# Kernel tuning notes

Hardware: AMD Instinct MI355X
Metric: run time of the kernel (lower is better)

The kernel has to match this reference:

```python
import jax, jax.numpy as jnp
import numpy as np

B, T = 256, 2048
K_LABELS = 50
K2 = K_LABELS + 2  # includes START (K) and STOP (K+1) tags
NEG_INF = -10000.0


def setup_inputs() -> dict:
    key = jax.random.key(0)
    k1, k2, k3, k4 = jax.random.split(key, 4)
    emissions = jax.random.normal(k1, (B, T, K2), dtype=jnp.float32)
    transitions = jax.random.normal(k2, (K2, K2), dtype=jnp.float32)
    lengths = jax.random.randint(k3, (B,), 1, T + 1, dtype=jnp.int64)
    labels = jax.random.randint(k4, (B, T), 0, K_LABELS, dtype=jnp.int64)
    return {"emissions": emissions, "transitions": transitions,
            "lengths": lengths, "labels": labels}


def _forward_algo(emissions, transitions, lengths):
    b, t, k2 = emissions.shape
    start_tag, stop_tag = k2 - 2, k2 - 1
    init = jnp.full((k2,), NEG_INF, emissions.dtype).at[start_tag].set(0.0)
    alpha0 = jnp.broadcast_to(init, (b, k2))  # [B, K2]

    def step(alpha, emit):
        # tag_var[b, next, prev] = emit[b, next] + trans[next, prev] + alpha[b, prev]
        tag_var = emit[:, :, None] + transitions[None, :, :] + alpha[:, None, :]
        new_alpha = jax.nn.logsumexp(tag_var, axis=2)  # [B, K2]
        return new_alpha, new_alpha

    _, alphas = jax.lax.scan(step, alpha0, jnp.swapaxes(emissions, 0, 1))
    all_alphas = jnp.concatenate([alpha0[None], alphas], axis=0)  # [T+1, B, K2]
    fv = all_alphas[lengths, jnp.arange(b)]  # alpha at each sequence's final step
    terminal = fv + transitions[stop_tag][None, :]
    return jax.nn.logsumexp(terminal, axis=1)  # [B]


def _score_label(emissions, transitions, lengths, labels):
    b, t, k2 = emissions.shape
    start_tag, stop_tag = k2 - 2, k2 - 1
    start_col = jnp.full((b, 1), start_tag, labels.dtype)
    stop_col = jnp.full((b, 1), stop_tag, labels.dtype)
    pad_start = jnp.concatenate([start_col, labels], axis=1)  # [B, T+1]
    pad_stop = jnp.concatenate([labels, stop_col], axis=1)    # [B, T+1]
    pos = jnp.arange(t + 1)
    pad_stop = jnp.where(pos[None, :] >= lengths[:, None], stop_tag, pad_stop)
    # transition score over positions 0..length (inclusive)
    trans_mask = pos[None, :] <= lengths[:, None]
    trans_sc = jnp.where(trans_mask, transitions[pad_stop, pad_start], 0.0).sum(axis=1)
    # emission score over positions 0..length-1
    emit_mask = jnp.arange(t)[None, :] < lengths[:, None]
    emit_vals = jnp.take_along_axis(emissions, labels[..., None], axis=-1)[..., 0]
    emit_sc = jnp.where(emit_mask, emit_vals, 0.0).sum(axis=1)
    return trans_sc + emit_sc  # [B]


def reference(emissions, transitions, lengths, labels):
    forward_score = _forward_algo(emissions, transitions, lengths)
    gold_score = _score_label(emissions, transitions, lengths, labels)
    return jnp.mean(forward_score - gold_score)
```

## Files before the change

### kernel.cpp

```cpp
#include <hip/hip_runtime.h>


#define B_    256
#define T_    2048
#define K2_   52
#define LOG2E_ 1.4426950408889634f
#define LN2_   0.6931471805599453f

__device__ __forceinline__ float rdlane(float v, int src) {
  return __uint_as_float(__builtin_amdgcn_readlane(__float_as_uint(v), src));
}
__device__ __forceinline__ int imin(int a, int b) { return a < b ? a : b; }
__device__ __forceinline__ int imax(int a, int b) { return a > b ? a : b; }

#define FORALL52(F) \
  F(0,0) F(1,1) F(2,2) F(3,3) F(4,0) F(5,1) F(6,2) F(7,3) \
  F(8,0) F(9,1) F(10,2) F(11,3) F(12,0) F(13,1) F(14,2) F(15,3) \
  F(16,0) F(17,1) F(18,2) F(19,3) F(20,0) F(21,1) F(22,2) F(23,3) \
  F(24,0) F(25,1) F(26,2) F(27,3) F(28,0) F(29,1) F(30,2) F(31,3) \
  F(32,0) F(33,1) F(34,2) F(35,3) F(36,0) F(37,1) F(38,2) F(39,3) \
  F(40,0) F(41,1) F(42,2) F(43,3) F(48,0) F(49,1) F(50,2) F(51,3) \
  F(44,0) F(45,1) F(46,2) F(47,3)

#define DECLM_F(i, c) float M_##i = __builtin_amdgcn_exp2f(tr[n * K2_ + i] * LOG2E_);
#define DECLM_B(i, c) float M_##i = __builtin_amdgcn_exp2f(tr[i * K2_ + n] * LOG2E_);
#define ACCF(i, c)  _a##c = fmaf(M_##i, rdlane(_src, i), _a##c);

#define MATVEC(OUTY) \
    float _a0 = 0.0f, _a1 = 0.0f, _a2 = 0.0f, _a3 = 0.0f; \
    FORALL52(ACCF) \
    float OUTY = (_a0 + _a1) + (_a2 + _a3);

#define FSTEP_R(EV, NEWIDX) do {                                \
    float _ne  = emb[(NEWIDX) * K2_ + n];                       \
    float _m   = rdlane(vv, 50);                                \
    float _inv = __builtin_amdgcn_rcpf(_m);                     \
    C += __builtin_amdgcn_logf(_m);                             \
    float _E = __builtin_amdgcn_exp2f((EV) * LOG2E_);           \
    float _src = vv;                                            \
    MATVEC(_y)                                                  \
    vv = _y * _inv * _E;                                        \
    EV = _ne;                                                   \
  } while (0)
#define FSTEP_N(EV, NEWIDX) do {                                \
    float _ne  = emb[(NEWIDX) * K2_ + n];                       \
    float _E = __builtin_amdgcn_exp2f((EV) * LOG2E_);           \
    float _src = vv;                                            \
    MATVEC(_y)                                                  \
    vv = _y * _E;                                               \
    EV = _ne;                                                   \
  } while (0)

#define BSTEP_R(EV, NEWIDX) do {                                \
    float _ne  = emb[(NEWIDX) * K2_ + n];                       \
    float _m   = rdlane(vv, 0);                                 \
    float _inv = __builtin_amdgcn_rcpf(_m);                     \
    C += __builtin_amdgcn_logf(_m);                             \
    float _E = __builtin_amdgcn_exp2f((EV) * LOG2E_);           \
    float _src = vv * _E;                                       \
    MATVEC(_y)                                                  \
    vv = _y * _inv;                                             \
    EV = _ne;                                                   \
  } while (0)
#define BSTEP_N(EV, NEWIDX) do {                                \
    float _ne  = emb[(NEWIDX) * K2_ + n];                       \
    float _E = __builtin_amdgcn_exp2f((EV) * LOG2E_);           \
    float _src = vv * _E;                                       \
    MATVEC(_y)                                                  \
    vv = _y;                                                    \
    EV = _ne;                                                   \
  } while (0)

#define PIN(a,b,c,d,e,f,g,h,i,j,k,l,m) \
  asm volatile("" : "+v"(M_##a), "+v"(M_##b), "+v"(M_##c), "+v"(M_##d), \
                    "+v"(M_##e), "+v"(M_##f), "+v"(M_##g), "+v"(M_##h), \
                    "+v"(M_##i), "+v"(M_##j), "+v"(M_##k), "+v"(M_##l), \
                    "+v"(M_##m));
#define PIN_ALL \
  PIN( 0, 1, 2, 3, 4, 5, 6, 7, 8, 9,10,11,12) \
  PIN(13,14,15,16,17,18,19,20,21,22,23,24,25) \
  PIN(26,27,28,29,30,31,32,33,34,35,36,37,38) \
  PIN(39,40,41,42,43,44,45,46,47,48,49,50,51)

__launch_bounds__(128, 1)
__global__ void crf_fwd_kernel(const float* __restrict__ em,
                               const float* __restrict__ tr,
                               const int*  __restrict__ len,
                               const int*  __restrict__ lab,
                               float* __restrict__ per_b)
{
  const int b    = blockIdx.x;
  const int tid  = threadIdx.x;
  const int wave = tid >> 6;
  const int lane = tid & 63;
  const int n    = (lane < K2_) ? lane : (K2_ - 1);
  const int L    = len[b];
  const int h    = L >> 1;
  const float* emb = em + (size_t)b * (T_ * K2_);

  __shared__ float sU[64];
  __shared__ float sCb[1];
  __shared__ float sG[2];

  float vv, C = 0.0f;

  if (wave == 0) {
    FORALL52(DECLM_F)
    PIN_ALL
    vv = (lane == 50) ? 1.0f : 0.0f;
    float e0 = emb[0 * K2_ + n];
    float e1 = emb[1 * K2_ + n];
    float e2 = emb[2 * K2_ + n];
    float e3 = emb[3 * K2_ + n];
    int t = 0;
    for (; t + 4 <= h; t += 4) {
      int i4 = imin(t + 4, T_ - 1), i5 = imin(t + 5, T_ - 1);
      int i6 = imin(t + 6, T_ - 1), i7 = imin(t + 7, T_ - 1);
      FSTEP_R(e0, i4);
      FSTEP_N(e1, i5);
      FSTEP_N(e2, i6);
      FSTEP_N(e3, i7);
    }
    int rem = h - t;
    if (rem > 0) FSTEP_R(e0, T_ - 1);
    if (rem > 1) FSTEP_N(e1, T_ - 1);
    if (rem > 2) FSTEP_N(e2, T_ - 1);
  } else {
    FORALL52(DECLM_B)
    PIN_ALL
    vv = __builtin_amdgcn_exp2f(tr[(K2_ - 1) * K2_ + n] * LOG2E_);
    int cnt = L - h;
    float e0 = emb[(L - 1) * K2_ + n];
    float e1 = emb[imax(L - 2, 0) * K2_ + n];
    float e2 = emb[imax(L - 3, 0) * K2_ + n];
    float e3 = emb[imax(L - 4, 0) * K2_ + n];
    int s = 0;
    for (; s + 4 <= cnt; s += 4) {
      int j4 = imax(L - 5 - s, 0), j5 = imax(L - 6 - s, 0);
      int j6 = imax(L - 7 - s, 0), j7 = imax(L - 8 - s, 0);
      BSTEP_R(e0, j4);
      BSTEP_N(e1, j5);
      BSTEP_N(e2, j6);
      BSTEP_N(e3, j7);
    }
    int rem = cnt - s;
    if (rem > 0) BSTEP_R(e0, 0);
    if (rem > 1) BSTEP_N(e1, 0);
    if (rem > 2) BSTEP_N(e2, 0);

    sU[lane] = vv;
    if (lane == 0) sCb[0] = C;
  }

  float gold = 0.0f;
  const int* labb = lab + b * T_;
  for (int tt = tid; tt < L; tt += 128) {
    int l1 = labb[tt];
    int l0 = (tt == 0) ? 50 : labb[tt - 1];
    gold += emb[tt * K2_ + l1] + tr[l1 * K2_ + l0];
  }
  if (tid == 0) gold += tr[(K2_ - 1) * K2_ + labb[L - 1]];
#pragma unroll
  for (int off = 32; off >= 1; off >>= 1)
    gold += __shfl_xor(gold, off, 64);
  if (lane == 0) sG[wave] = gold;

  __syncthreads();

  if (wave == 0) {
    float x = (lane < K2_) ? vv * sU[lane] : 0.0f;
#pragma unroll
    for (int off = 32; off >= 1; off >>= 1)
      x += __shfl_xor(x, off, 64);
    float fwd = (C + sCb[0] + __builtin_amdgcn_logf(x)) * LN2_;
    if (lane == 0) per_b[b] = fwd - (sG[0] + sG[1]);
  }
}

__global__ void reduce_mean_kernel(const float* __restrict__ per_b,
                                   float* __restrict__ out)
{
  const int tid = threadIdx.x;
  float v = per_b[tid];
#pragma unroll
  for (int off = 32; off >= 1; off >>= 1) v += __shfl_xor(v, off, 64);
  __shared__ float s[4];
  if ((tid & 63) == 0) s[tid >> 6] = v;
  __syncthreads();
  if (tid == 0) out[0] = ((s[0] + s[1]) + (s[2] + s[3])) * (1.0f / (float)B_);
}

extern "C" void kernel_launch(void* const* d_in, const int* in_sizes, int n_in,
                              void* d_out, int out_size, void* d_ws, size_t ws_size,
                              hipStream_t stream) {
  const float* em  = (const float*)d_in[0];
  const float* tr  = (const float*)d_in[1];
  const int*   len = (const int*)d_in[2];
  const int*   lab = (const int*)d_in[3];
  float* out = (float*)d_out;
  float* ws  = (float*)d_ws;

  crf_fwd_kernel<<<B_, 128, 0, stream>>>(em, tr, len, lab, ws);
  reduce_mean_kernel<<<1, 256, 0, stream>>>(ws, out);
}
```

Baseline: 424.9 us.

## Broadcast CRF state via LDS float4 reads instead of per-lane readlane

Each recurrence step now writes the 52-element state vector to a per-wave shared-memory buffer. Every lane then reads it back as 13 broadcast float4 loads, replacing 52 v_readlane scalar broadcasts per step. The renormalisation value comes from the loaded vector. The backward wave's emission pre-scaling is shifted so the exponential is applied before the store, which adds one prefetched emission register. This trades SALU/readlane serialization for LDS write-read latency on the sequential critical path, relying on in-wave ordering without barriers.

Result: faster. 399.2 us (-6.0%).

```diff
diff --git a/kernel.cpp b/kernel.cpp
--- a/kernel.cpp
+++ b/kernel.cpp
@@ -7,69 +7,18 @@
 #define LOG2E_ 1.4426950408889634f
 #define LN2_   0.6931471805599453f
 
-__device__ __forceinline__ float rdlane(float v, int src) {
-  return __uint_as_float(__builtin_amdgcn_readlane(__float_as_uint(v), src));
-}
 __device__ __forceinline__ int imin(int a, int b) { return a < b ? a : b; }
 __device__ __forceinline__ int imax(int a, int b) { return a > b ? a : b; }
 
 #define FORALL52(F) \
-  F(0,0) F(1,1) F(2,2) F(3,3) F(4,0) F(5,1) F(6,2) F(7,3) \
-  F(8,0) F(9,1) F(10,2) F(11,3) F(12,0) F(13,1) F(14,2) F(15,3) \
-  F(16,0) F(17,1) F(18,2) F(19,3) F(20,0) F(21,1) F(22,2) F(23,3) \
-  F(24,0) F(25,1) F(26,2) F(27,3) F(28,0) F(29,1) F(30,2) F(31,3) \
-  F(32,0) F(33,1) F(34,2) F(35,3) F(36,0) F(37,1) F(38,2) F(39,3) \
-  F(40,0) F(41,1) F(42,2) F(43,3) F(48,0) F(49,1) F(50,2) F(51,3) \
-  F(44,0) F(45,1) F(46,2) F(47,3)
-
-#define DECLM_F(i, c) float M_##i = __builtin_amdgcn_exp2f(tr[n * K2_ + i] * LOG2E_);
-#define DECLM_B(i, c) float M_##i = __builtin_amdgcn_exp2f(tr[i * K2_ + n] * LOG2E_);
-#define ACCF(i, c)  _a##c = fmaf(M_##i, rdlane(_src, i), _a##c);
-
-#define MATVEC(OUTY) \
-    float _a0 = 0.0f, _a1 = 0.0f, _a2 = 0.0f, _a3 = 0.0f; \
-    FORALL52(ACCF) \
-    float OUTY = (_a0 + _a1) + (_a2 + _a3);
-
-#define FSTEP_R(EV, NEWIDX) do {                                \
-    float _ne  = emb[(NEWIDX) * K2_ + n];                       \
-    float _m   = rdlane(vv, 50);                                \
-    float _inv = __builtin_amdgcn_rcpf(_m);                     \
-    C += __builtin_amdgcn_logf(_m);                             \
-    float _E = __builtin_amdgcn_exp2f((EV) * LOG2E_);           \
-    float _src = vv;                                            \
-    MATVEC(_y)                                                  \
-    vv = _y * _inv * _E;                                        \
-    EV = _ne;                                                   \
-  } while (0)
-#define FSTEP_N(EV, NEWIDX) do {                                \
-    float _ne  = emb[(NEWIDX) * K2_ + n];                       \
-    float _E = __builtin_amdgcn_exp2f((EV) * LOG2E_);           \
-    float _src = vv;                                            \
-    MATVEC(_y)                                                  \
-    vv = _y * _E;                                               \
-    EV = _ne;                                                   \
-  } while (0)
-
-#define BSTEP_R(EV, NEWIDX) do {                                \
-    float _ne  = emb[(NEWIDX) * K2_ + n];                       \
-    float _m   = rdlane(vv, 0);                                 \
-    float _inv = __builtin_amdgcn_rcpf(_m);                     \
-    C += __builtin_amdgcn_logf(_m);                             \
-    float _E = __builtin_amdgcn_exp2f((EV) * LOG2E_);           \
-    float _src = vv * _E;                                       \
-    MATVEC(_y)                                                  \
-    vv = _y * _inv;                                             \
-    EV = _ne;                                                   \
-  } while (0)
-#define BSTEP_N(EV, NEWIDX) do {                                \
-    float _ne  = emb[(NEWIDX) * K2_ + n];                       \
-    float _E = __builtin_amdgcn_exp2f((EV) * LOG2E_);           \
-    float _src = vv * _E;                                       \
-    MATVEC(_y)                                                  \
-    vv = _y;                                                    \
-    EV = _ne;                                                   \
-  } while (0)
+  F(0) F(1) F(2) F(3) F(4) F(5) F(6) F(7) F(8) F(9) F(10) F(11) F(12) F(13) \
+  F(14) F(15) F(16) F(17) F(18) F(19) F(20) F(21) F(22) F(23) F(24) F(25) \
+  F(26) F(27) F(28) F(29) F(30) F(31) F(32) F(33) F(34) F(35) F(36) F(37) \
+  F(38) F(39) F(40) F(41) F(42) F(43) F(44) F(45) F(46) F(47) F(48) F(49) \
+  F(50) F(51)
+
+#define DECLM_F(i) float M_##i = __builtin_amdgcn_exp2f(tr[n * K2_ + i] * LOG2E_);
+#define DECLM_B(i) float M_##i = __builtin_amdgcn_exp2f(tr[i * K2_ + n] * LOG2E_);
 
 #define PIN(a,b,c,d,e,f,g,h,i,j,k,l,m) \
   asm volatile("" : "+v"(M_##a), "+v"(M_##b), "+v"(M_##c), "+v"(M_##d), \
@@ -81,6 +30,79 @@
   PIN(13,14,15,16,17,18,19,20,21,22,23,24,25) \
   PIN(26,27,28,29,30,31,32,33,34,35,36,37,38) \
   PIN(39,40,41,42,43,44,45,46,47,48,49,50,51)
+
+#define ACCQ(Q, i0,i1,i2,i3) \
+  _a0 = fmaf(M_##i0, (Q).x, _a0); \
+  _a1 = fmaf(M_##i1, (Q).y, _a1); \
+  _a2 = fmaf(M_##i2, (Q).z, _a2); \
+  _a3 = fmaf(M_##i3, (Q).w, _a3);
+
+#define ACC_ALL \
+  ACCQ(_q0 , 0, 1, 2, 3)  ACCQ(_q1 , 4, 5, 6, 7)  ACCQ(_q2 , 8, 9,10,11) \
+  ACCQ(_q3 ,12,13,14,15)  ACCQ(_q4 ,16,17,18,19)  ACCQ(_q5 ,20,21,22,23) \
+  ACCQ(_q6 ,24,25,26,27)  ACCQ(_q7 ,28,29,30,31)  ACCQ(_q8 ,32,33,34,35) \
+  ACCQ(_q9 ,36,37,38,39)  ACCQ(_q10,40,41,42,43)  ACCQ(_q11,44,45,46,47) \
+  ACCQ(_qc ,48,49,50,51)
+
+#define MATVEC_F(OUTY, RENORMV) \
+    const float4* _g4 = (const float4*)sh; \
+    float4 _qc  = _g4[12]; \
+    float4 _q0  = _g4[0],  _q1  = _g4[1],  _q2  = _g4[2],  _q3  = _g4[3]; \
+    float4 _q4  = _g4[4],  _q5  = _g4[5],  _q6  = _g4[6],  _q7  = _g4[7]; \
+    float4 _q8  = _g4[8],  _q9  = _g4[9],  _q10 = _g4[10], _q11 = _g4[11]; \
+    float RENORMV = _qc.z; (void)RENORMV; \
+    float _a0 = 0.0f, _a1 = 0.0f, _a2 = 0.0f, _a3 = 0.0f; \
+    ACC_ALL \
+    float OUTY = (_a0 + _a1) + (_a2 + _a3);
+
+#define MATVEC_B(OUTY, RENORMV) \
+    const float4* _g4 = (const float4*)sh; \
+    float4 _q0  = _g4[0]; \
+    float4 _q1  = _g4[1],  _q2  = _g4[2],  _q3  = _g4[3],  _q4  = _g4[4]; \
+    float4 _q5  = _g4[5],  _q6  = _g4[6],  _q7  = _g4[7],  _q8  = _g4[8]; \
+    float4 _q9  = _g4[9],  _q10 = _g4[10], _q11 = _g4[11], _qc  = _g4[12]; \
+    float RENORMV = _q0.x; (void)RENORMV; \
+    float _a0 = 0.0f, _a1 = 0.0f, _a2 = 0.0f, _a3 = 0.0f; \
+    ACC_ALL \
+    float OUTY = (_a0 + _a1) + (_a2 + _a3);
+
+#define FSTEP_R(EV, NEWIDX) do {                                \
+    float _ne  = emb[(size_t)(NEWIDX) * K2_ + n];               \
+    MATVEC_F(_y, _m)                                            \
+    float _inv = __builtin_amdgcn_rcpf(_m);                     \
+    C += __builtin_amdgcn_logf(_m);                             \
+    float _E = __builtin_amdgcn_exp2f((EV) * LOG2E_);           \
+    vv = _y * (_inv * _E);                                      \
+    sh[lane] = vv;                                              \
+    EV = _ne;                                                   \
+  } while (0)
+#define FSTEP_N(EV, NEWIDX) do {                                \
+    float _ne  = emb[(size_t)(NEWIDX) * K2_ + n];               \
+    MATVEC_F(_y, _mu)                                           \
+    float _E = __builtin_amdgcn_exp2f((EV) * LOG2E_);           \
+    vv = _y * _E;                                               \
+    sh[lane] = vv;                                              \
+    EV = _ne;                                                   \
+  } while (0)
+
+#define BSTEP_R(EV, NEWIDX) do {                                \
+    float _ne  = emb[(size_t)(NEWIDX) * K2_ + n];               \
+    MATVEC_B(_y, _m)                                            \
+    float _inv = __builtin_amdgcn_rcpf(_m);                     \
+    C += __builtin_amdgcn_logf(_m);                             \
+    vv = _y * _inv;                                             \
+    float _E = __builtin_amdgcn_exp2f((EV) * LOG2E_);           \
+    sh[lane] = vv * _E;                                         \
+    EV = _ne;                                                   \
+  } while (0)
+#define BSTEP_N(EV, NEWIDX) do {                                \
+    float _ne  = emb[(size_t)(NEWIDX) * K2_ + n];               \
+    MATVEC_B(_y, _mu)                                           \
+    vv = _y;                                                    \
+    float _E = __builtin_amdgcn_exp2f((EV) * LOG2E_);           \
+    sh[lane] = vv * _E;                                         \
+    EV = _ne;                                                   \
+  } while (0)
 
 __launch_bounds__(128, 1)
 __global__ void crf_fwd_kernel(const float* __restrict__ em,
@@ -98,16 +120,18 @@
   const int h    = L >> 1;
   const float* emb = em + (size_t)b * (T_ * K2_);
 
-  __shared__ float sU[64];
+  __shared__ __align__(16) float sV[2][64];
   __shared__ float sCb[1];
   __shared__ float sG[2];
 
+  float* sh = sV[wave];
   float vv, C = 0.0f;
 
   if (wave == 0) {
     FORALL52(DECLM_F)
     PIN_ALL
     vv = (lane == 50) ? 1.0f : 0.0f;
+    sh[lane] = vv;
     float e0 = emb[0 * K2_ + n];
     float e1 = emb[1 * K2_ + n];
     float e2 = emb[2 * K2_ + n];
@@ -130,25 +154,27 @@
     PIN_ALL
     vv = __builtin_amdgcn_exp2f(tr[(K2_ - 1) * K2_ + n] * LOG2E_);
     int cnt = L - h;
-    float e0 = emb[(L - 1) * K2_ + n];
-    float e1 = emb[imax(L - 2, 0) * K2_ + n];
-    float e2 = emb[imax(L - 3, 0) * K2_ + n];
-    float e3 = emb[imax(L - 4, 0) * K2_ + n];
+    float e0 = emb[(size_t)(L - 1) * K2_ + n];
+    float eA = emb[(size_t)imax(L - 2, 0) * K2_ + n];
+    float eB = emb[(size_t)imax(L - 3, 0) * K2_ + n];
+    float eC = emb[(size_t)imax(L - 4, 0) * K2_ + n];
+    float eD = emb[(size_t)imax(L - 5, 0) * K2_ + n];
+    sh[lane] = vv * __builtin_amdgcn_exp2f(e0 * LOG2E_);
     int s = 0;
     for (; s + 4 <= cnt; s += 4) {
-      int j4 = imax(L - 5 - s, 0), j5 = imax(L - 6 - s, 0);
-      int j6 = imax(L - 7 - s, 0), j7 = imax(L - 8 - s, 0);
-      BSTEP_R(e0, j4);
-      BSTEP_N(e1, j5);
-      BSTEP_N(e2, j6);
-      BSTEP_N(e3, j7);
+      int j4 = imax(L - 6 - s, 0), j5 = imax(L - 7 - s, 0);
+      int j6 = imax(L - 8 - s, 0), j7 = imax(L - 9 - s, 0);
+      BSTEP_R(eA, j4);
+      BSTEP_N(eB, j5);
+      BSTEP_N(eC, j6);
+      BSTEP_N(eD, j7);
     }
     int rem = cnt - s;
-    if (rem > 0) BSTEP_R(e0, 0);
-    if (rem > 1) BSTEP_N(e1, 0);
-    if (rem > 2) BSTEP_N(e2, 0);
-
-    sU[lane] = vv;
+    if (rem > 0) BSTEP_R(eA, 0);
+    if (rem > 1) BSTEP_N(eB, 0);
+    if (rem > 2) BSTEP_N(eC, 0);
+
+    sh[lane] = vv;
     if (lane == 0) sCb[0] = C;
   }
 
@@ -157,7 +183,7 @@
   for (int tt = tid; tt < L; tt += 128) {
     int l1 = labb[tt];
     int l0 = (tt == 0) ? 50 : labb[tt - 1];
-    gold += emb[tt * K2_ + l1] + tr[l1 * K2_ + l0];
+    gold += emb[(size_t)tt * K2_ + l1] + tr[l1 * K2_ + l0];
   }
   if (tid == 0) gold += tr[(K2_ - 1) * K2_ + labb[L - 1]];
 #pragma unroll
@@ -168,7 +194,7 @@
   __syncthreads();
 
   if (wave == 0) {
-    float x = (lane < K2_) ? vv * sU[lane] : 0.0f;
+    float x = (lane < K2_) ? vv * sV[1][lane] : 0.0f;
 #pragma unroll
     for (int off = 32; off >= 1; off >>= 1)
       x += __shfl_xor(x, off, 64);
```

## Pair length-sorted sequences per block and matvec via LDS float4 reads

Applied to the files above, without the earlier changes.

Adds a bitonic sort of sequence lengths so each block processes two sequences of similar length, interleaving their forward (and backward) recurrences to hide latency, and halves the grid to 128 blocks. The per-step matvec now broadcasts the state vector through shared memory with float4 reads instead of 52 readlane instructions, using 8 accumulators. This trades an extra sort launch and LDS round trips per step for more independent work per wave; the two interleaved chains should cover each other's dependency latency, but unmatched tails still run serially.

New measurement: 529.6 us. 1.25x slower.

```diff
diff --git a/kernel.cpp b/kernel.cpp
--- a/kernel.cpp
+++ b/kernel.cpp
@@ -7,173 +7,363 @@
 #define LOG2E_ 1.4426950408889634f
 #define LN2_   0.6931471805599453f
 
-__device__ __forceinline__ float rdlane(float v, int src) {
-  return __uint_as_float(__builtin_amdgcn_readlane(__float_as_uint(v), src));
-}
 __device__ __forceinline__ int imin(int a, int b) { return a < b ? a : b; }
 __device__ __forceinline__ int imax(int a, int b) { return a > b ? a : b; }
 
+#define X2F(e) __builtin_amdgcn_exp2f((e) * LOG2E_)
+
 #define FORALL52(F) \
-  F(0,0) F(1,1) F(2,2) F(3,3) F(4,0) F(5,1) F(6,2) F(7,3) \
-  F(8,0) F(9,1) F(10,2) F(11,3) F(12,0) F(13,1) F(14,2) F(15,3) \
-  F(16,0) F(17,1) F(18,2) F(19,3) F(20,0) F(21,1) F(22,2) F(23,3) \
-  F(24,0) F(25,1) F(26,2) F(27,3) F(28,0) F(29,1) F(30,2) F(31,3) \
-  F(32,0) F(33,1) F(34,2) F(35,3) F(36,0) F(37,1) F(38,2) F(39,3) \
-  F(40,0) F(41,1) F(42,2) F(43,3) F(48,0) F(49,1) F(50,2) F(51,3) \
-  F(44,0) F(45,1) F(46,2) F(47,3)
-
-#define DECLM_F(i, c) float M_##i = __builtin_amdgcn_exp2f(tr[n * K2_ + i] * LOG2E_);
-#define DECLM_B(i, c) float M_##i = __builtin_amdgcn_exp2f(tr[i * K2_ + n] * LOG2E_);
-#define ACCF(i, c)  _a##c = fmaf(M_##i, rdlane(_src, i), _a##c);
-
-#define MATVEC(OUTY) \
-    float _a0 = 0.0f, _a1 = 0.0f, _a2 = 0.0f, _a3 = 0.0f; \
-    FORALL52(ACCF) \
-    float OUTY = (_a0 + _a1) + (_a2 + _a3);
-
-#define FSTEP_R(EV, NEWIDX) do {                                \
-    float _ne  = emb[(NEWIDX) * K2_ + n];                       \
-    float _m   = rdlane(vv, 50);                                \
-    float _inv = __builtin_amdgcn_rcpf(_m);                     \
-    C += __builtin_amdgcn_logf(_m);                             \
-    float _E = __builtin_amdgcn_exp2f((EV) * LOG2E_);           \
-    float _src = vv;                                            \
-    MATVEC(_y)                                                  \
-    vv = _y * _inv * _E;                                        \
-    EV = _ne;                                                   \
-  } while (0)
-#define FSTEP_N(EV, NEWIDX) do {                                \
-    float _ne  = emb[(NEWIDX) * K2_ + n];                       \
-    float _E = __builtin_amdgcn_exp2f((EV) * LOG2E_);           \
-    float _src = vv;                                            \
-    MATVEC(_y)                                                  \
-    vv = _y * _E;                                               \
-    EV = _ne;                                                   \
-  } while (0)
-
-#define BSTEP_R(EV, NEWIDX) do {                                \
-    float _ne  = emb[(NEWIDX) * K2_ + n];                       \
-    float _m   = rdlane(vv, 0);                                 \
-    float _inv = __builtin_amdgcn_rcpf(_m);                     \
-    C += __builtin_amdgcn_logf(_m);                             \
-    float _E = __builtin_amdgcn_exp2f((EV) * LOG2E_);           \
-    float _src = vv * _E;                                       \
-    MATVEC(_y)                                                  \
-    vv = _y * _inv;                                             \
-    EV = _ne;                                                   \
-  } while (0)
-#define BSTEP_N(EV, NEWIDX) do {                                \
-    float _ne  = emb[(NEWIDX) * K2_ + n];                       \
-    float _E = __builtin_amdgcn_exp2f((EV) * LOG2E_);           \
-    float _src = vv * _E;                                       \
-    MATVEC(_y)                                                  \
-    vv = _y;                                                    \
-    EV = _ne;                                                   \
-  } while (0)
-
-#define PIN(a,b,c,d,e,f,g,h,i,j,k,l,m) \
-  asm volatile("" : "+v"(M_##a), "+v"(M_##b), "+v"(M_##c), "+v"(M_##d), \
-                    "+v"(M_##e), "+v"(M_##f), "+v"(M_##g), "+v"(M_##h), \
-                    "+v"(M_##i), "+v"(M_##j), "+v"(M_##k), "+v"(M_##l), \
-                    "+v"(M_##m));
-#define PIN_ALL \
-  PIN( 0, 1, 2, 3, 4, 5, 6, 7, 8, 9,10,11,12) \
-  PIN(13,14,15,16,17,18,19,20,21,22,23,24,25) \
-  PIN(26,27,28,29,30,31,32,33,34,35,36,37,38) \
-  PIN(39,40,41,42,43,44,45,46,47,48,49,50,51)
-
-__launch_bounds__(128, 1)
-__global__ void crf_fwd_kernel(const float* __restrict__ em,
-                               const float* __restrict__ tr,
-                               const int*  __restrict__ len,
-                               const int*  __restrict__ lab,
-                               float* __restrict__ per_b)
+  F(0) F(1) F(2) F(3) F(4) F(5) F(6) F(7) F(8) F(9) F(10) F(11) F(12) F(13) \
+  F(14) F(15) F(16) F(17) F(18) F(19) F(20) F(21) F(22) F(23) F(24) F(25) \
+  F(26) F(27) F(28) F(29) F(30) F(31) F(32) F(33) F(34) F(35) F(36) F(37) \
+  F(38) F(39) F(40) F(41) F(42) F(43) F(44) F(45) F(46) F(47) F(48) F(49) \
+  F(50) F(51)
+
+#define DECLMF(i) float MF_##i; { float _t = tr[n * K2_ + i] * LOG2E_; \
+  asm volatile("v_exp_f32 %0, %1\n\ts_nop 1" : "=v"(MF_##i) : "v"(_t)); }
+#define DECLMB(i) float MB_##i; { float _t = tr[i * K2_ + n] * LOG2E_; \
+  asm volatile("v_exp_f32 %0, %1\n\ts_nop 1" : "=v"(MB_##i) : "v"(_t)); }
+
+#define READ13F(P, SH) \
+  const float4* P##g = (const float4*)(SH); \
+  float4 P##qc = P##g[12]; \
+  float4 P##q0 = P##g[0],  P##q1 = P##g[1],  P##q2  = P##g[2],  P##q3  = P##g[3]; \
+  float4 P##q4 = P##g[4],  P##q5 = P##g[5],  P##q6  = P##g[6],  P##q7  = P##g[7]; \
+  float4 P##q8 = P##g[8],  P##q9 = P##g[9],  P##q10 = P##g[10], P##q11 = P##g[11];
+
+#define READ13B(P, SH) \
+  const float4* P##g = (const float4*)(SH); \
+  float4 P##q0 = P##g[0],  P##q1 = P##g[1],  P##q2  = P##g[2],  P##q3  = P##g[3]; \
+  float4 P##q4 = P##g[4],  P##q5 = P##g[5],  P##q6  = P##g[6],  P##q7  = P##g[7]; \
+  float4 P##q8 = P##g[8],  P##q9 = P##g[9],  P##q10 = P##g[10], P##q11 = P##g[11]; \
+  float4 P##qc = P##g[12];
+
+#define ACCQ4(MP, Q, i0,i1,i2,i3, A0,A1,A2,A3) \
+  A0 = fmaf(MP##_##i0, (Q).x, A0); \
+  A1 = fmaf(MP##_##i1, (Q).y, A1); \
+  A2 = fmaf(MP##_##i2, (Q).z, A2); \
+  A3 = fmaf(MP##_##i3, (Q).w, A3);
+
+#define ACC52F(P) \
+  float P##s0=0.f,P##s1=0.f,P##s2=0.f,P##s3=0.f; \
+  float P##s4=0.f,P##s5=0.f,P##s6=0.f,P##s7=0.f; \
+  ACCQ4(MF, P##qc, 48,49,50,51, P##s0,P##s1,P##s2,P##s3) \
+  ACCQ4(MF, P##q0,  0, 1, 2, 3, P##s4,P##s5,P##s6,P##s7) \
+  ACCQ4(MF, P##q1,  4, 5, 6, 7, P##s0,P##s1,P##s2,P##s3) \
+  ACCQ4(MF, P##q2,  8, 9,10,11, P##s4,P##s5,P##s6,P##s7) \
+  ACCQ4(MF, P##q3, 12,13,14,15, P##s0,P##s1,P##s2,P##s3) \
+  ACCQ4(MF, P##q4, 16,17,18,19, P##s4,P##s5,P##s6,P##s7) \
+  ACCQ4(MF, P##q5, 20,21,22,23, P##s0,P##s1,P##s2,P##s3) \
+  ACCQ4(MF, P##q6, 24,25,26,27, P##s4,P##s5,P##s6,P##s7) \
+  ACCQ4(MF, P##q7, 28,29,30,31, P##s0,P##s1,P##s2,P##s3) \
+  ACCQ4(MF, P##q8, 32,33,34,35, P##s4,P##s5,P##s6,P##s7) \
+  ACCQ4(MF, P##q9, 36,37,38,39, P##s0,P##s1,P##s2,P##s3) \
+  ACCQ4(MF, P##q10,40,41,42,43, P##s4,P##s5,P##s6,P##s7) \
+  ACCQ4(MF, P##q11,44,45,46,47, P##s0,P##s1,P##s2,P##s3) \
+  float P##y = ((P##s0+P##s1)+(P##s2+P##s3)) + ((P##s4+P##s5)+(P##s6+P##s7));
+
+#define ACC52B(P) \
+  float P##s0=0.f,P##s1=0.f,P##s2=0.f,P##s3=0.f; \
+  float P##s4=0.f,P##s5=0.f,P##s6=0.f,P##s7=0.f; \
+  ACCQ4(MB, P##q0,  0, 1, 2, 3, P##s0,P##s1,P##s2,P##s3) \
+  ACCQ4(MB, P##q1,  4, 5, 6, 7, P##s4,P##s5,P##s6,P##s7) \
+  ACCQ4(MB, P##q2,  8, 9,10,11, P##s0,P##s1,P##s2,P##s3) \
+  ACCQ4(MB, P##q3, 12,13,14,15, P##s4,P##s5,P##s6,P##s7) \
+  ACCQ4(MB, P##q4, 16,17,18,19, P##s0,P##s1,P##s2,P##s3) \
+  ACCQ4(MB, P##q5, 20,21,22,23, P##s4,P##s5,P##s6,P##s7) \
+  ACCQ4(MB, P##q6, 24,25,26,27, P##s0,P##s1,P##s2,P##s3) \
+  ACCQ4(MB, P##q7, 28,29,30,31, P##s4,P##s5,P##s6,P##s7) \
+  ACCQ4(MB, P##q8, 32,33,34,35, P##s0,P##s1,P##s2,P##s3) \
+  ACCQ4(MB, P##q9, 36,37,38,39, P##s4,P##s5,P##s6,P##s7) \
+  ACCQ4(MB, P##q10,40,41,42,43, P##s0,P##s1,P##s2,P##s3) \
+  ACCQ4(MB, P##q11,44,45,46,47, P##s4,P##s5,P##s6,P##s7) \
+  ACCQ4(MB, P##qc, 48,49,50,51, P##s0,P##s1,P##s2,P##s3) \
+  float P##y = ((P##s0+P##s1)+(P##s2+P##s3)) + ((P##s4+P##s5)+(P##s6+P##s7));
+
+#define FSTEP2_R(EVA, NIA, EA, EVB, NIB, EB) do {                 \
+    float _neA = embA[(size_t)(NIA) * K2_ + n];                   \
+    float _neB = embB[(size_t)(NIB) * K2_ + n];                   \
+    READ13F(A, sF0)                                               \
+    READ13F(B, sF1)                                               \
+    ACC52F(A)                                                     \
+    { float _m = Aqc.z;                                           \
+      CfA += __builtin_amdgcn_logf(_m);                           \
+      vfA = Ay * (__builtin_amdgcn_rcpf(_m) * (EA));              \
+      sF0[lane] = vfA; }                                          \
+    EVA = _neA;                                                   \
+    ACC52F(B)                                                     \
+    { float _m = Bqc.z;                                           \
+      CfB += __builtin_amdgcn_logf(_m);                           \
+      vfB = By * (__builtin_amdgcn_rcpf(_m) * (EB));              \
+      sF1[lane] = vfB; }                                          \
+    EVB = _neB;                                                   \
+  } while (0)
+
+#define FSTEP2_N(EVA, NIA, EA, EVB, NIB, EB) do {                 \
+    float _neA = embA[(size_t)(NIA) * K2_ + n];                   \
+    float _neB = embB[(size_t)(NIB) * K2_ + n];                   \
+    READ13F(A, sF0)                                               \
+    READ13F(B, sF1)                                               \
+    ACC52F(A)                                                     \
+    vfA = Ay * (EA); sF0[lane] = vfA; EVA = _neA;                 \
+    ACC52F(B)                                                     \
+    vfB = By * (EB); sF1[lane] = vfB; EVB = _neB;                 \
+  } while (0)
+
+#define BSTEP2_R(EVA, NIA, EA, EVB, NIB, EB) do {                 \
+    float _neA = embA[(size_t)(NIA) * K2_ + n];                   \
+    float _neB = embB[(size_t)(NIB) * K2_ + n];                   \
+    READ13B(A, sB0)                                               \
+    READ13B(B, sB1)                                               \
+    ACC52B(A)                                                     \
+    { float _m = Aq0.x;                                           \
+      CbA += __builtin_amdgcn_logf(_m);                           \
+      vbA = Ay * __builtin_amdgcn_rcpf(_m);                       \
+      sB0[lane] = vbA * (EA); }                                   \
+    EVA = _neA;                                                   \
+    ACC52B(B)                                                     \
+    { float _m = Bq0.x;                                           \
+      CbB += __builtin_amdgcn_logf(_m);                           \
+      vbB = By * __builtin_amdgcn_rcpf(_m);                       \
+      sB1[lane] = vbB * (EB); }                                   \
+    EVB = _neB;                                                   \
+  } while (0)
+
+#define BSTEP2_N(EVA, NIA, EA, EVB, NIB, EB) do {                 \
+    float _neA = embA[(size_t)(NIA) * K2_ + n];                   \
+    float _neB = embB[(size_t)(NIB) * K2_ + n];                   \
+    READ13B(A, sB0)                                               \
+    READ13B(B, sB1)                                               \
+    ACC52B(A)                                                     \
+    vbA = Ay; sB0[lane] = vbA * (EA); EVA = _neA;                 \
+    ACC52B(B)                                                     \
+    vbB = By; sB1[lane] = vbB * (EB); EVB = _neB;                 \
+  } while (0)
+
+#define FSOLO_R(SH, VV, CC, EV, NI, EMB) do {                     \
+    float _ne = EMB[(size_t)(NI) * K2_ + n];                      \
+    READ13F(S, SH)                                                \
+    ACC52F(S)                                                     \
+    float _m = Sqc.z;                                             \
+    CC += __builtin_amdgcn_logf(_m);                              \
+    VV = Sy * (__builtin_amdgcn_rcpf(_m) * X2F(EV));              \
+    SH[lane] = VV; EV = _ne;                                      \
+  } while (0)
+#define FSOLO_N(SH, VV, EV, NI, EMB) do {                         \
+    float _ne = EMB[(size_t)(NI) * K2_ + n];                      \
+    READ13F(S, SH)                                                \
+    ACC52F(S)                                                     \
+    VV = Sy * X2F(EV);                                            \
+    SH[lane] = VV; EV = _ne;                                      \
+  } while (0)
+#define BSOLO_R(SH, VV, CC, EV, NI, EMB) do {                     \
+    float _ne = EMB[(size_t)(NI) * K2_ + n];                      \
+    READ13B(S, SH)                                                \
+    ACC52B(S)                                                     \
+    float _m = Sq0.x;                                             \
+    CC += __builtin_amdgcn_logf(_m);                              \
+    VV = Sy * __builtin_amdgcn_rcpf(_m);                          \
+    SH[lane] = VV * X2F(EV); EV = _ne;                            \
+  } while (0)
+#define BSOLO_N(SH, VV, EV, NI, EMB) do {                         \
+    float _ne = EMB[(size_t)(NI) * K2_ + n];                      \
+    READ13B(S, SH)                                                \
+    ACC52B(S)                                                     \
+    VV = Sy;                                                      \
+    SH[lane] = VV * X2F(EV); EV = _ne;                            \
+  } while (0)
+
+__global__ void pair_kernel(const int* __restrict__ len, int* __restrict__ perm)
 {
-  const int b    = blockIdx.x;
+  __shared__ int sk[256], sv[256];
+  const int tid = threadIdx.x;
+  sk[tid] = len[tid]; sv[tid] = tid;
+  __syncthreads();
+  for (int size = 2; size <= 256; size <<= 1) {
+    for (int j = size >> 1; j > 0; j >>= 1) {
+      int ixj = tid ^ j;
+      if (ixj > tid) {
+        int a = sk[tid], b2 = sk[ixj];
+        bool up = ((tid & size) == 0);
+        if (up ? (a > b2) : (a < b2)) {
+          sk[tid] = b2; sk[ixj] = a;
+          int tv = sv[tid]; sv[tid] = sv[ixj]; sv[ixj] = tv;
+        }
+      }
+      __syncthreads();
+    }
+  }
+  perm[tid] = sv[tid];
+}
+
+__global__ __launch_bounds__(128)
+__attribute__((amdgpu_waves_per_eu(1, 1)))
+void crf_fwd_kernel(const float* __restrict__ em,
+                    const float* __restrict__ tr,
+                    const int*  __restrict__ len,
+                    const int*  __restrict__ lab,
+                    const int*  __restrict__ perm,
+                    float* __restrict__ per_b)
+{
   const int tid  = threadIdx.x;
   const int wave = tid >> 6;
   const int lane = tid & 63;
   const int n    = (lane < K2_) ? lane : (K2_ - 1);
-  const int L    = len[b];
-  const int h    = L >> 1;
-  const float* emb = em + (size_t)b * (T_ * K2_);
-
-  __shared__ float sU[64];
-  __shared__ float sCb[1];
+  const int pA   = perm[2 * blockIdx.x];
+  const int pB   = perm[2 * blockIdx.x + 1];
+  const int LA   = len[pA], LB = len[pB];
+  const int hA   = LA >> 1, hB = LB >> 1;
+  const float* embA = em + (size_t)pA * (T_ * K2_);
+  const float* embB = em + (size_t)pB * (T_ * K2_);
+
+  __shared__ __align__(16) float sF0[64], sF1[64];
+  __shared__ __align__(16) float sB0[64], sB1[64];
+  __shared__ float sC[2];
   __shared__ float sG[2];
 
-  float vv, C = 0.0f;
+  float vfA = 0.f, vfB = 0.f, CfA = 0.f, CfB = 0.f;
 
   if (wave == 0) {
-    FORALL52(DECLM_F)
-    PIN_ALL
-    vv = (lane == 50) ? 1.0f : 0.0f;
-    float e0 = emb[0 * K2_ + n];
-    float e1 = emb[1 * K2_ + n];
-    float e2 = emb[2 * K2_ + n];
-    float e3 = emb[3 * K2_ + n];
+    FORALL52(DECLMF)
+    vfA = (lane == 50) ? 1.0f : 0.0f;
+    vfB = vfA;
+    sF0[lane] = vfA; sF1[lane] = vfB;
+    float fA0 = embA[0 * K2_ + n], fA1 = embA[1 * K2_ + n];
+    float fA2 = embA[2 * K2_ + n], fA3 = embA[3 * K2_ + n];
+    float fB0 = embB[0 * K2_ + n], fB1 = embB[1 * K2_ + n];
+    float fB2 = embB[2 * K2_ + n], fB3 = embB[3 * K2_ + n];
+
+    const int mn = imin(hA, hB);
     int t = 0;
-    for (; t + 4 <= h; t += 4) {
-      int i4 = imin(t + 4, T_ - 1), i5 = imin(t + 5, T_ - 1);
-      int i6 = imin(t + 6, T_ - 1), i7 = imin(t + 7, T_ - 1);
-      FSTEP_R(e0, i4);
-      FSTEP_N(e1, i5);
-      FSTEP_N(e2, i6);
-      FSTEP_N(e3, i7);
-    }
-    int rem = h - t;
-    if (rem > 0) FSTEP_R(e0, T_ - 1);
-    if (rem > 1) FSTEP_N(e1, T_ - 1);
-    if (rem > 2) FSTEP_N(e2, T_ - 1);
+    for (; t + 4 <= mn; t += 4) {
+      float EA0 = X2F(fA0), EA1 = X2F(fA1), EA2 = X2F(fA2), EA3 = X2F(fA3);
+      float EB0 = X2F(fB0), EB1 = X2F(fB1), EB2 = X2F(fB2), EB3 = X2F(fB3);
+      int iA4 = imin(t + 4, T_ - 1), iA5 = imin(t + 5, T_ - 1);
+      int iA6 = imin(t + 6, T_ - 1), iA7 = imin(t + 7, T_ - 1);
+      FSTEP2_R(fA0, iA4, EA0, fB0, iA4, EB0);
+      FSTEP2_N(fA1, iA5, EA1, fB1, iA5, EB1);
+      FSTEP2_N(fA2, iA6, EA2, fB2, iA6, EB2);
+      FSTEP2_N(fA3, iA7, EA3, fB3, iA7, EB3);
+    }
+    int tA = t;
+    while (tA + 4 <= hA) {
+      FSOLO_R(sF0, vfA, CfA, fA0, imin(tA + 4, T_ - 1), embA);
+      FSOLO_N(sF0, vfA,      fA1, imin(tA + 5, T_ - 1), embA);
+      FSOLO_N(sF0, vfA,      fA2, imin(tA + 6, T_ - 1), embA);
+      FSOLO_N(sF0, vfA,      fA3, imin(tA + 7, T_ - 1), embA);
+      tA += 4;
+    }
+    int remA = hA - tA;
+    if (remA > 0) FSOLO_R(sF0, vfA, CfA, fA0, T_ - 1, embA);
+    if (remA > 1) FSOLO_N(sF0, vfA,      fA1, T_ - 1, embA);
+    if (remA > 2) FSOLO_N(sF0, vfA,      fA2, T_ - 1, embA);
+    int tB = t;
+    while (tB + 4 <= hB) {
+      FSOLO_R(sF1, vfB, CfB, fB0, imin(tB + 4, T_ - 1), embB);
+      FSOLO_N(sF1, vfB,      fB1, imin(tB + 5, T_ - 1), embB);
+      FSOLO_N(sF1, vfB,      fB2, imin(tB + 6, T_ - 1), embB);
+      FSOLO_N(sF1, vfB,      fB3, imin(tB + 7, T_ - 1), embB);
+      tB += 4;
+    }
+    int remB = hB - tB;
+    if (remB > 0) FSOLO_R(sF1, vfB, CfB, fB0, T_ - 1, embB);
+    if (remB > 1) FSOLO_N(sF1, vfB,      fB1, T_ - 1, embB);
+    if (remB > 2) FSOLO_N(sF1, vfB,      fB2, T_ - 1, embB);
   } else {
-    FORALL52(DECLM_B)
-    PIN_ALL
-    vv = __builtin_amdgcn_exp2f(tr[(K2_ - 1) * K2_ + n] * LOG2E_);
-    int cnt = L - h;
-    float e0 = emb[(L - 1) * K2_ + n];
-    float e1 = emb[imax(L - 2, 0) * K2_ + n];
-    float e2 = emb[imax(L - 3, 0) * K2_ + n];
-    float e3 = emb[imax(L - 4, 0) * K2_ + n];
+    FORALL52(DECLMB)
+    float vbA, vbB, CbA = 0.f, CbB = 0.f;
+    vbA = __builtin_amdgcn_exp2f(tr[(K2_ - 1) * K2_ + n] * LOG2E_);
+    vbB = vbA;
+    const int cA = LA - hA, cB = LB - hB;
+    float eA0 = embA[(size_t)(LA - 1) * K2_ + n];
+    float eB0 = embB[(size_t)(LB - 1) * K2_ + n];
+    float bA0 = embA[(size_t)imax(LA - 2, 0) * K2_ + n];
+    float bA1 = embA[(size_t)imax(LA - 3, 0) * K2_ + n];
+    float bA2 = embA[(size_t)imax(LA - 4, 0) * K2_ + n];
+    float bA3 = embA[(size_t)imax(LA - 5, 0) * K2_ + n];
+    float bB0 = embB[(size_t)imax(LB - 2, 0) * K2_ + n];
+    float bB1 = embB[(size_t)imax(LB - 3, 0) * K2_ + n];
+    float bB2 = embB[(size_t)imax(LB - 4, 0) * K2_ + n];
+    float bB3 = embB[(size_t)imax(LB - 5, 0) * K2_ + n];
+    sB0[lane] = vbA * X2F(eA0);
+    sB1[lane] = vbB * X2F(eB0);
+
+    const int mc = imin(cA, cB);
     int s = 0;
-    for (; s + 4 <= cnt; s += 4) {
-      int j4 = imax(L - 5 - s, 0), j5 = imax(L - 6 - s, 0);
-      int j6 = imax(L - 7 - s, 0), j7 = imax(L - 8 - s, 0);
-      BSTEP_R(e0, j4);
-      BSTEP_N(e1, j5);
-      BSTEP_N(e2, j6);
-      BSTEP_N(e3, j7);
-    }
-    int rem = cnt - s;
-    if (rem > 0) BSTEP_R(e0, 0);
-    if (rem > 1) BSTEP_N(e1, 0);
-    if (rem > 2) BSTEP_N(e2, 0);
-
-    sU[lane] = vv;
-    if (lane == 0) sCb[0] = C;
+    for (; s + 4 <= mc; s += 4) {
+      float EA0 = X2F(bA0), EA1 = X2F(bA1), EA2 = X2F(bA2), EA3 = X2F(bA3);
+      float EB0 = X2F(bB0), EB1 = X2F(bB1), EB2 = X2F(bB2), EB3 = X2F(bB3);
+      int jA4 = imax(LA - 6 - s, 0), jA5 = imax(LA - 7 - s, 0);
+      int jA6 = imax(LA - 8 - s, 0), jA7 = imax(LA - 9 - s, 0);
+      int jB4 = imax(LB - 6 - s, 0), jB5 = imax(LB - 7 - s, 0);
+      int jB6 = imax(LB - 8 - s, 0), jB7 = imax(LB - 9 - s, 0);
+      BSTEP2_R(bA0, jA4, EA0, bB0, jB4, EB0);
+      BSTEP2_N(bA1, jA5, EA1, bB1, jB5, EB1);
+      BSTEP2_N(bA2, jA6, EA2, bB2, jB6, EB2);
+      BSTEP2_N(bA3, jA7, EA3, bB3, jB7, EB3);
+    }
+    int sA = s;
+    while (sA + 4 <= cA) {
+      BSOLO_R(sB0, vbA, CbA, bA0, imax(LA - 6 - sA, 0), embA);
+      BSOLO_N(sB0, vbA,      bA1, imax(LA - 7 - sA, 0), embA);
+      BSOLO_N(sB0, vbA,      bA2, imax(LA - 8 - sA, 0), embA);
+      BSOLO_N(sB0, vbA,      bA3, imax(LA - 9 - sA, 0), embA);
+      sA += 4;
+    }
+    int remA = cA - sA;
+    if (remA > 0) BSOLO_R(sB0, vbA, CbA, bA0, 0, embA);
+    if (remA > 1) BSOLO_N(sB0, vbA,      bA1, 0, embA);
+    if (remA > 2) BSOLO_N(sB0, vbA,      bA2, 0, embA);
+    int sB_ = s;
+    while (sB_ + 4 <= cB) {
+      BSOLO_R(sB1, vbB, CbB, bB0, imax(LB - 6 - sB_, 0), embB);
+      BSOLO_N(sB1, vbB,      bB1, imax(LB - 7 - sB_, 0), embB);
+      BSOLO_N(sB1, vbB,      bB2, imax(LB - 8 - sB_, 0), embB);
+      BSOLO_N(sB1, vbB,      bB3, imax(LB - 9 - sB_, 0), embB);
+      sB_ += 4;
+    }
+    int remB = cB - sB_;
+    if (remB > 0) BSOLO_R(sB1, vbB, CbB, bB0, 0, embB);
+    if (remB > 1) BSOLO_N(sB1, vbB,      bB1, 0, embB);
+    if (remB > 2) BSOLO_N(sB1, vbB,      bB2, 0, embB);
+
+    sB0[lane] = vbA;
+    sB1[lane] = vbB;
+    if (lane == 0) { sC[0] = CbA; sC[1] = CbB; }
   }
 
-  float gold = 0.0f;
-  const int* labb = lab + b * T_;
-  for (int tt = tid; tt < L; tt += 128) {
-    int l1 = labb[tt];
-    int l0 = (tt == 0) ? 50 : labb[tt - 1];
-    gold += emb[tt * K2_ + l1] + tr[l1 * K2_ + l0];
-  }
-  if (tid == 0) gold += tr[(K2_ - 1) * K2_ + labb[L - 1]];
-#pragma unroll
-  for (int off = 32; off >= 1; off >>= 1)
-    gold += __shfl_xor(gold, off, 64);
-  if (lane == 0) sG[wave] = gold;
-
-  __syncthreads();
-
-  if (wave == 0) {
-    float x = (lane < K2_) ? vv * sU[lane] : 0.0f;
+  {
+    const int    pg   = (wave == 0) ? pA : pB;
+    const int    Lg   = (wave == 0) ? LA : LB;
+    const float* embG = (wave == 0) ? embA : embB;
+    const int*   labb = lab + pg * T_;
+    float gold = 0.0f;
+    for (int tt = lane; tt < Lg; tt += 64) {
+      int l1 = labb[tt];
+      int l0 = (tt == 0) ? 50 : labb[tt - 1];
+      gold += embG[(size_t)tt * K2_ + l1] + tr[l1 * K2_ + l0];
+    }
+    if (lane == 0) gold += tr[(K2_ - 1) * K2_ + labb[Lg - 1]];
 #pragma unroll
     for (int off = 32; off >= 1; off >>= 1)
-      x += __shfl_xor(x, off, 64);
-    float fwd = (C + sCb[0] + __builtin_amdgcn_logf(x)) * LN2_;
-    if (lane == 0) per_b[b] = fwd - (sG[0] + sG[1]);
+      gold += __shfl_xor(gold, off, 64);
+    if (lane == 0) sG[wave] = gold;
+  }
+
+  __syncthreads();
+
+  if (wave == 0) {
+    float xA = (lane < K2_) ? vfA * sB0[lane] : 0.0f;
+    float xB = (lane < K2_) ? vfB * sB1[lane] : 0.0f;
+#pragma unroll
+    for (int off = 32; off >= 1; off >>= 1) {
+      xA += __shfl_xor(xA, off, 64);
+      xB += __shfl_xor(xB, off, 64);
+    }
+    if (lane == 0) {
+      per_b[pA] = (CfA + sC[0] + __builtin_amdgcn_logf(xA)) * LN2_ - sG[0];
+      per_b[pB] = (CfB + sC[1] + __builtin_amdgcn_logf(xB)) * LN2_ - sG[1];
+    }
   }
 }
 
@@ -197,9 +387,11 @@
   const float* tr  = (const float*)d_in[1];
   const int*   len = (const int*)d_in[2];
   const int*   lab = (const int*)d_in[3];
-  float* out = (float*)d_out;
-  float* ws  = (float*)d_ws;
-
-  crf_fwd_kernel<<<B_, 128, 0, stream>>>(em, tr, len, lab, ws);
+  float* out  = (float*)d_out;
+  float* ws   = (float*)d_ws;
+  int*   perm = (int*)(ws + B_);
+
+  pair_kernel<<<1, 256, 0, stream>>>(len, perm);
+  crf_fwd_kernel<<<B_ / 2, 128, 0, stream>>>(em, tr, len, lab, perm, ws);
   reduce_mean_kernel<<<1, 256, 0, stream>>>(ws, out);
 }
```
